# Optimization experiments

Measured on AMD Instinct MI355X. Metric: run time of the kernel, lower is better.

## Reference

```python
import jax, jax.numpy as jnp
import numpy as np

# Degree-sorted atom layout (DeepChem convention): atoms of degree d are contiguous.
D_COUNTS = [8192, 65536, 131072, 196608, 98304, 16384, 8192]  # degrees 0..6
OFFSETS = np.cumsum([0] + D_COUNTS)  # start index of each degree block
N_ATOMS = int(OFFSETS[-1])           # 524288
F_IN = 75
BATCH = 16384
MAX_DEG = 6
BN_EPS = 1e-3


def setup_inputs() -> dict:
    key = jax.random.key(0)
    ks = jax.random.split(key, 40)
    inp = {}
    inp["atom_features"] = jax.random.normal(ks[0], (N_ATOMS, F_IN), jnp.float32)
    # every molecule gets exactly N_ATOMS/BATCH atoms -> all segments populated
    inp["membership"] = (jnp.arange(N_ATOMS, dtype=jnp.int32) % BATCH)
    for d in range(1, MAX_DEG + 1):
        inp[f"adj{d}"] = jax.random.randint(ks[d], (D_COUNTS[d], d), 0, N_ATOMS, dtype=jnp.int32)
    # GraphConv weights: 2*MAX_DEG + 1 = 13 matrices (rel/self per degree 1..6, self for degree 0)
    inp["gc1_W"] = jax.random.normal(ks[10], (13, F_IN, 32), jnp.float32) * 0.1
    inp["gc1_b"] = jax.random.normal(ks[11], (13, 32), jnp.float32) * 0.01
    inp["gc2_W"] = jax.random.normal(ks[12], (13, 32, 32), jnp.float32) * 0.1
    inp["gc2_b"] = jax.random.normal(ks[13], (13, 32), jnp.float32) * 0.01
    inp["bn1_gamma"] = jnp.ones((32,), jnp.float32)
    inp["bn1_beta"] = jnp.zeros((32,), jnp.float32)
    inp["bn1_mean"] = jax.random.normal(ks[14], (32,), jnp.float32) * 0.1
    inp["bn1_var"] = jax.random.uniform(ks[15], (32,), jnp.float32, 0.5, 1.5)
    inp["bn3_gamma"] = jnp.ones((64,), jnp.float32)
    inp["bn3_beta"] = jnp.zeros((64,), jnp.float32)
    inp["bn3_mean"] = jax.random.normal(ks[16], (64,), jnp.float32) * 0.1
    inp["bn3_var"] = jax.random.uniform(ks[17], (64,), jnp.float32, 0.5, 1.5)
    inp["d1_W"] = jax.random.normal(ks[18], (32, 64), jnp.float32) * 0.1
    inp["d1_b"] = jnp.zeros((64,), jnp.float32)
    inp["d2_W"] = jax.random.normal(ks[19], (128, 1), jnp.float32) * 0.1
    inp["d2_b"] = jnp.zeros((1,), jnp.float32)
    inp["d3_W"] = jnp.array([0.5, -1, -1, 1, 1, 1, 1, 1, -1, -1, -1, -1, -1, -1, -1, -1], jnp.float32)[:, None]
    inp["d3_b"] = jnp.zeros((1,), jnp.float32)
    inp["x_add"] = jax.random.normal(ks[20], (BATCH, 15), jnp.float32)
    inp["batch_size"] = BATCH
    return inp


def _batch_norm(x, gamma, beta, mean, var):
    return gamma * (x - mean) * jax.lax.rsqrt(var + BN_EPS) + beta


def _graph_conv(atoms, adjs, W, b):
    # atoms: [N, F]; adjs[d-1]: [n_d, d] neighbor indices for degree-d atoms
    outs = []
    for d in range(1, MAX_DEG + 1):
        s, n = int(OFFSETS[d]), D_COUNTS[d]
        rel = atoms[adjs[d - 1]].sum(axis=1)          # [n_d, F] summed neighbors
        self_a = atoms[s:s + n]                        # [n_d, F]
        wr, br = W[2 * (d - 1)], b[2 * (d - 1)]
        ws, bs = W[2 * (d - 1) + 1], b[2 * (d - 1) + 1]
        outs.append(rel @ wr + br + self_a @ ws + bs)
    out0 = atoms[:D_COUNTS[0]] @ W[12] + b[12]         # degree-0: self only
    return jnp.tanh(jnp.concatenate([out0] + outs, axis=0))


def _graph_pool(atoms, adjs):
    outs = [atoms[:D_COUNTS[0]]]  # degree-0 passthrough
    for d in range(1, MAX_DEG + 1):
        s, n = int(OFFSETS[d]), D_COUNTS[d]
        self_a = atoms[s:s + n]
        neigh_max = atoms[adjs[d - 1]].max(axis=1)     # [n_d, F]
        outs.append(jnp.maximum(self_a, neigh_max))    # max over {self} U neighbors
    return jnp.concatenate(outs, axis=0)


def reference(atom_features, membership, adj1, adj2, adj3, adj4, adj5, adj6,
              gc1_W, gc1_b, gc2_W, gc2_b,
              bn1_gamma, bn1_beta, bn1_mean, bn1_var,
              bn3_gamma, bn3_beta, bn3_mean, bn3_var,
              d1_W, d1_b, d2_W, d2_b, d3_W, d3_b, x_add, batch_size):
    adjs = [adj1, adj2, adj3, adj4, adj5, adj6]
    h = _graph_conv(atom_features, adjs, gc1_W, gc1_b)          # [N, 32], tanh
    h = _batch_norm(h, bn1_gamma, bn1_beta, bn1_mean, bn1_var)
    h = _graph_pool(h, adjs)
    h = _graph_conv(h, adjs, gc2_W, gc2_b)                      # [N, 32]
    # NOTE: original reuses batch_norm1 here (source does self.batch_norm1 twice)
    h = _batch_norm(h, bn1_gamma, bn1_beta, bn1_mean, bn1_var)
    h = _graph_pool(h, adjs)
    h = jnp.tanh(h @ d1_W + d1_b)                               # [N, 64]
    h = _batch_norm(h, bn3_gamma, bn3_beta, bn3_mean, bn3_var)
    # GraphGather: per-molecule sum and max readout
    sum_r = jax.ops.segment_sum(h, membership, num_segments=batch_size)
    max_r = jax.ops.segment_max(h, membership, num_segments=batch_size)
    mol = jnp.tanh(jnp.concatenate([sum_r, max_r], axis=1))     # [B, 128]
    model_var = mol @ d2_W + d2_b                               # [B, 1]
    binding = jnp.concatenate([model_var, x_add], axis=1)       # [B, 16]
    ans = binding @ d3_W + d3_b                                 # [B, 1]
    return ans.reshape(1, -1)
```

## Files before the change

kernel.cpp:

```cpp
#include <hip/hip_runtime.h>

typedef unsigned short u16;
typedef __bf16 bf8v __attribute__((ext_vector_type(8)));
typedef float f32x4 __attribute__((ext_vector_type(4)));

#define N_ATOMS 524288
#define NROW32  16777216

#define P_EP1   0
#define P_EP2   224
#define P_BN1   448
#define P_BN3   576
#define P_D1WT  832
#define P_D1B   2880
#define P_D2W   2944
#define P_SC    3072

__device__ __forceinline__ float b2f(u16 u) {
  return __builtin_bit_cast(float, ((unsigned)u) << 16);
}
__device__ __forceinline__ u16 f2b(float f) {
  unsigned x = __builtin_bit_cast(unsigned, f);
  x += 0x7fffu + ((x >> 16) & 1u);
  return (u16)(x >> 16);
}
__device__ __forceinline__ float ldf(const void* p, size_t i, int isbf) {
  return isbf ? b2f(((const u16*)p)[i]) : ((const float*)p)[i];
}
__device__ __forceinline__ u16 ldb(const void* p, size_t i, int isbf) {
  return isbf ? ((const u16*)p)[i] : f2b(((const float*)p)[i]);
}

__device__ __forceinline__ float exp2_fast(float x) {
#if __has_builtin(__builtin_amdgcn_exp2f)
  return __builtin_amdgcn_exp2f(x);
#else
  return exp2f(x);
#endif
}
__device__ __forceinline__ float rcp_fast(float x) {
#if __has_builtin(__builtin_amdgcn_rcpf)
  return __builtin_amdgcn_rcpf(x);
#else
  return 1.0f / x;
#endif
}
__device__ __forceinline__ float tanh_fast(float x) {
  float xc = fminf(fmaxf(x, -15.f), 15.f);
  float t = exp2_fast(xc * -2.8853900817779268f);
  return (1.f - t) * rcp_fast(1.f + t);
}

__device__ __forceinline__ void seg_of(int r, int& d, int& off) {
  if      (r < 8192)   { d = 0; off = 0; }
  else if (r < 73728)  { d = 1; off = 8192; }
  else if (r < 204800) { d = 2; off = 73728; }
  else if (r < 401408) { d = 3; off = 204800; }
  else if (r < 499712) { d = 4; off = 401408; }
  else if (r < 516096) { d = 5; off = 499712; }
  else                 { d = 6; off = 516096; }
}

__global__ void probe_kernel(const void* __restrict__ atoms, int* __restrict__ flag) {
  int lane = threadIdx.x;
  unsigned u = ((const u16*)atoms)[(size_t)lane * 148];
  int e = (u >> 7) & 0xFF;
  bool ok = (e >= 100 && e <= 140);
  unsigned long long b = __ballot(ok);
  if (lane == 0) flag[0] = (__popcll(b) >= 48) ? 1 : 0;
}

__global__ __launch_bounds__(64) void prep_kernel(
    const void* gW1, const void* gB1, const void* gW2, const void* gB2,
    const void* b1g, const void* b1b, const void* b1m, const void* b1v,
    const void* g3, const void* b3, const void* m3, const void* v3,
    const void* d1W, const void* d1b, const void* d2W, const void* d2b,
    const void* d3W, const void* d3b,
    const int* flagp, char* ws)
{
  const int isbf = flagp[0];
  const int lane = threadIdx.x;
  float* P  = (float*)(ws + 256);
  u16* wf1 = (u16*)(ws + 16384);
  u16* wf2 = (u16*)(ws + 88064);
  const int blk = blockIdx.x;

  if (blk < 7) {
    const int d = blk;
    const int wr  = (d == 0) ? 12 : 2 * (d - 1);
    const int wsi = (d == 0) ? 12 : 2 * (d - 1) + 1;
    const int nl = lane & 15, q = lane >> 4;
    #pragma unroll
    for (int ks = 0; ks < 5; ++ks)
      #pragma unroll
      for (int ct = 0; ct < 2; ++ct) {
        u16* dst = wf1 + (size_t)(((d * 5 + ks) * 2 + ct) * 64 + lane) * 8;
        #pragma unroll
        for (int j = 0; j < 8; ++j) {
          int k = ks * 32 + q * 8 + j, n = ct * 16 + nl;
          u16 val = 0;
          if (k < 75) val = ldb(gW1, (size_t)wr * 2400 + k * 32 + n, isbf);
          else if (k >= 80 && k < 155) val = ldb(gW1, (size_t)wsi * 2400 + (k - 80) * 32 + n, isbf);
          dst[j] = val;
        }
      }
    #pragma unroll
    for (int ks = 0; ks < 2; ++ks)
      #pragma unroll
      for (int ct = 0; ct < 2; ++ct) {
        u16* dst = wf2 + (size_t)(((d * 2 + ks) * 2 + ct) * 64 + lane) * 8;
        #pragma unroll
        for (int j = 0; j < 8; ++j) {
          int k = ks * 32 + q * 8 + j, n = ct * 16 + nl;
          dst[j] = (k < 32) ? ldb(gW2, (size_t)wr * 1024 + k * 32 + n, isbf)
                            : ldb(gW2, (size_t)wsi * 1024 + (k - 32) * 32 + n, isbf);
        }
      }
    if (lane < 32) {
      int col = lane;
      float bb1 = (d == 0) ? ldf(gB1, 12 * 32 + col, isbf)
                           : ldf(gB1, wr * 32 + col, isbf) + ldf(gB1, wsi * 32 + col, isbf);
      float bb2 = (d == 0) ? ldf(gB2, 12 * 32 + col, isbf)
                           : ldf(gB2, wr * 32 + col, isbf) + ldf(gB2, wsi * 32 + col, isbf);
      P[P_EP1 + d * 32 + col] = bb1;
      P[P_EP2 + d * 32 + col] = bb2;
    }
  } else {
    if (lane < 32) {
      P[P_BN1 + lane]      = ldf(b1g, lane, isbf);
      P[P_BN1 + 32 + lane] = ldf(b1b, lane, isbf);
      P[P_BN1 + 64 + lane] = ldf(b1m, lane, isbf);
      P[P_BN1 + 96 + lane] = 1.0f / sqrtf(ldf(b1v, lane, isbf) + 0.001f);
    }
    P[P_BN3 + lane]       = ldf(g3, lane, isbf);
    P[P_BN3 + 64 + lane]  = ldf(b3, lane, isbf);
    P[P_BN3 + 128 + lane] = ldf(m3, lane, isbf);
    P[P_BN3 + 192 + lane] = 1.0f / sqrtf(ldf(v3, lane, isbf) + 0.001f);
    for (int k = 0; k < 32; ++k)
      P[P_D1WT + lane * 32 + k] = ldf(d1W, k * 64 + lane, isbf);
    P[P_D1B + lane] = ldf(d1b, lane, isbf);
    P[P_D2W + lane]      = ldf(d2W, lane, isbf);
    P[P_D2W + 64 + lane] = ldf(d2W, 64 + lane, isbf);
    if (lane < 16) P[P_SC + 1 + lane] = ldf(d3W, lane, isbf);
    if (lane == 0) { P[P_SC] = ldf(d2b, 0, isbf); P[P_SC + 17] = ldf(d3b, 0, isbf); }
  }
}

__global__ __launch_bounds__(256) void convert_kernel(
    const void* __restrict__ atoms, const int* flagp, u16* __restrict__ outB)
{
  __shared__ __align__(16) u16 sT[128 * 80];
  const int isbf = flagp[0];
  const int tid = threadIdx.x;
  const int rb = blockIdx.x * 128;

  for (int i = tid; i < 128 * 5; i += 256) {
    int rl = i / 5, k = 75 + (i % 5);
    sT[rl * 80 + k] = 0;
  }
  if (isbf) {
    const uint4* in4 = (const uint4*)((const u16*)atoms + (size_t)rb * 75);
    for (int i = tid; i < 1200; i += 256) {
      union { uint4 u4; u16 us[8]; } w; w.u4 = in4[i];
      int e0 = i * 8;
      #pragma unroll
      for (int j = 0; j < 8; ++j) {
        int e = e0 + j, rl = e / 75, k = e - rl * 75;
        sT[rl * 80 + k] = w.us[j];
      }
    }
  } else {
    const f32x4* in4 = (const f32x4*)((const float*)atoms + (size_t)rb * 75);
    for (int i = tid; i < 2400; i += 256) {
      f32x4 v = in4[i];
      int e0 = i * 4;
      #pragma unroll
      for (int j = 0; j < 4; ++j) {
        int e = e0 + j, rl = e / 75, k = e - rl * 75;
        sT[rl * 80 + k] = f2b(v[j]);
      }
    }
  }
  __syncthreads();
  uint4* dst = (uint4*)(outB + (size_t)rb * 80);
  const uint4* src = (const uint4*)sT;
  for (int i = tid; i < 1280; i += 256) dst[i] = src[i];
}

template<int D>
__device__ __forceinline__ void gather2_conv1(
    const u16* __restrict__ atomsB, const int* __restrict__ adjp,
    int r0, int r1, int off, int q, bf8v a0[5], bf8v a1[5])
{
  constexpr int DD = (D > 0) ? D : 1;
  int nb0[DD], nb1[DD];
  if (D > 0) {
    size_t i0 = (size_t)(r0 - off) * D, i1 = (size_t)(r1 - off) * D;
    #pragma unroll
    for (int j = 0; j < D; ++j) { nb0[j] = adjp[i0 + j]; nb1[j] = adjp[i1 + j]; }
  }
  const u16* s0 = atomsB + (size_t)r0 * 80;
  const u16* s1 = atomsB + (size_t)r1 * 80;
  #pragma unroll
  for (int ks = 0; ks < 5; ++ks) {
    const int c = ks * 32 + q * 8;
    if (c >= 80) {
      a0[ks] = *(const bf8v*)(s0 + (c - 80));
      a1[ks] = *(const bf8v*)(s1 + (c - 80));
    } else {
      uint4 v0[DD], v1[DD];
      #pragma unroll
      for (int j = 0; j < D; ++j) {
        v0[j] = *(const uint4*)(atomsB + (size_t)nb0[j] * 80 + c);
        v1[j] = *(const uint4*)(atomsB + (size_t)nb1[j] * 80 + c);
      }
      float r0s[8], r1s[8];
      #pragma unroll
      for (int i = 0; i < 8; ++i) { r0s[i] = 0.f; r1s[i] = 0.f; }
      #pragma unroll
      for (int j = 0; j < D; ++j) {
        union { uint4 u4; u16 us[8]; } a, b;
        a.u4 = v0[j]; b.u4 = v1[j];
        #pragma unroll
        for (int i = 0; i < 8; ++i) { r0s[i] += b2f(a.us[i]); r1s[i] += b2f(b.us[i]); }
      }
      union { u16 us[8]; bf8v v; } o0, o1;
      #pragma unroll
      for (int i = 0; i < 8; ++i) { o0.us[i] = f2b(r0s[i]); o1.us[i] = f2b(r1s[i]); }
      a0[ks] = o0.v; a1[ks] = o1.v;
    }
  }
}

__global__ __launch_bounds__(256) void conv1_fast_kernel(
    const u16* __restrict__ atomsB, const u16* __restrict__ wf1, const float* __restrict__ P,
    const int* __restrict__ a1p, const int* __restrict__ a2p, const int* __restrict__ a3p,
    const int* __restrict__ a4p, const int* __restrict__ a5p, const int* __restrict__ a6p,
    u16* __restrict__ out)
{
  const int tid = threadIdx.x;
  const int rb = blockIdx.x * 128;
  int d, off; seg_of(rb, d, off);
  const int lane = tid & 63;
  const int nl = lane & 15;
  const int q  = lane >> 4;
  const int wvid = tid >> 6;

  bf8v bfrag[5][2];
  #pragma unroll
  for (int ks = 0; ks < 5; ++ks)
    #pragma unroll
    for (int ct = 0; ct < 2; ++ct)
      bfrag[ks][ct] = *(const bf8v*)(wf1 + (size_t)(((d * 5 + ks) * 2 + ct) * 64 + lane) * 8);

  const int r0 = rb + wvid * 32 + nl;
  const int r1 = r0 + 16;
  bf8v a0[5], a1f[5];
  switch (d) {
    case 0: gather2_conv1<0>(atomsB, a1p, r0, r1, off, q, a0, a1f); break;
    case 1: gather2_conv1<1>(atomsB, a1p, r0, r1, off, q, a0, a1f); break;
    case 2: gather2_conv1<2>(atomsB, a2p, r0, r1, off, q, a0, a1f); break;
    case 3: gather2_conv1<3>(atomsB, a3p, r0, r1, off, q, a0, a1f); break;
    case 4: gather2_conv1<4>(atomsB, a4p, r0, r1, off, q, a0, a1f); break;
    case 5: gather2_conv1<5>(atomsB, a5p, r0, r1, off, q, a0, a1f); break;
    default: gather2_conv1<6>(atomsB, a6p, r0, r1, off, q, a0, a1f); break;
  }

  f32x4 acc[2][2] = {{{0,0,0,0},{0,0,0,0}},{{0,0,0,0},{0,0,0,0}}};
  #pragma unroll
  for (int ks = 0; ks < 5; ++ks) {
    acc[0][0] = __builtin_amdgcn_mfma_f32_16x16x32_bf16(a0[ks],  bfrag[ks][0], acc[0][0], 0, 0, 0);
    acc[0][1] = __builtin_amdgcn_mfma_f32_16x16x32_bf16(a0[ks],  bfrag[ks][1], acc[0][1], 0, 0, 0);
    acc[1][0] = __builtin_amdgcn_mfma_f32_16x16x32_bf16(a1f[ks], bfrag[ks][0], acc[1][0], 0, 0, 0);
    acc[1][1] = __builtin_amdgcn_mfma_f32_16x16x32_bf16(a1f[ks], bfrag[ks][1], acc[1][1], 0, 0, 0);
  }

  #pragma unroll
  for (int ct = 0; ct < 2; ++ct) {
    const int col = ct * 16 + nl;
    const float bias = P[P_EP1 + d * 32 + col];
    const float g  = P[P_BN1 + col];
    const float be = P[P_BN1 + 32 + col];
    const float mn = P[P_BN1 + 64 + col];
    const float iv = P[P_BN1 + 96 + col];
    #pragma unroll
    for (int t = 0; t < 2; ++t) {
      #pragma unroll
      for (int reg = 0; reg < 4; ++reg) {
        int row = rb + wvid * 32 + t * 16 + q * 4 + reg;
        float v = tanh_fast(acc[t][ct][reg] + bias);
        out[(size_t)row * 32 + col] = f2b(g * (v - mn) * iv + be);
      }
    }
  }
}

__global__ __launch_bounds__(256) void conv1_slow_kernel(
    const void* __restrict__ atoms, const void* __restrict__ gW, const void* __restrict__ gB,
    const void* __restrict__ bng, const void* __restrict__ bnb,
    const void* __restrict__ bnm, const void* __restrict__ bnv,
    const int* __restrict__ a1, const int* __restrict__ a2, const int* __restrict__ a3,
    const int* __restrict__ a4, const int* __restrict__ a5, const int* __restrict__ a6,
    const int* flagp, u16* __restrict__ out)
{
  __shared__ __align__(16) u16 sX[64 * 168];
  const int isbf = flagp[0];
  const int tid = threadIdx.x;
  const int rb = blockIdx.x * 64;
  int d, off; seg_of(rb, d, off);
  const int wr  = (d == 0) ? 12 : 2 * (d - 1);
  const int wsi = (d == 0) ? 12 : 2 * (d - 1) + 1;
  const size_t wrb = (size_t)wr  * 2400;
  const size_t wsb = (size_t)wsi * 2400;
  const int lane = tid & 63;
  const int nl = lane & 15;
  const int q  = lane >> 4;

  bf8v bfrag[5][2];
  #pragma unroll
  for (int ks = 0; ks < 5; ++ks)
    #pragma unroll
    for (int ct = 0; ct < 2; ++ct) {
      union { u16 u[8]; bf8v v; } tmp;
      #pragma unroll
      for (int j = 0; j < 8; ++j) {
        int k = ks * 32 + q * 8 + j, n = ct * 16 + nl;
        u16 val = 0;
        if (k < 75) val = ldb(gW, wrb + (size_t)k * 32 + n, isbf);
        else if (k >= 80 && k < 155) val = ldb(gW, wsb + (size_t)(k - 80) * 32 + n, isbf);
        tmp.u[j] = val;
      }
      bfrag[ks][ct] = tmp.v;
    }

  {
    const int lr = tid >> 2;
    const int kq = tid & 3;
    const int r  = rb + lr;
    int nb[6];
    if (d > 0) {
      const int* adjp = (d==1)?a1:(d==2)?a2:(d==3)?a3:(d==4)?a4:(d==5)?a5:a6;
      size_t ib = (size_t)(r - off) * d;
      for (int j = 0; j < d; ++j) nb[j] = adjp[ib + j];
    }
    u16* px = sX + lr * 168;
    for (int k = kq; k < 80; k += 4) {
      u16 sv = 0; float rs = 0.f;
      if (k < 75) {
        sv = ldb(atoms, (size_t)r * 75 + k, isbf);
        for (int j = 0; j < d; ++j) rs += ldf(atoms, (size_t)nb[j] * 75 + k, isbf);
      }
      px[80 + k] = sv;
      px[k]      = f2b(rs);
    }
  }
  __syncthreads();

  const int wvid = tid >> 6;
  f32x4 acc0 = {0.f, 0.f, 0.f, 0.f};
  f32x4 acc1 = {0.f, 0.f, 0.f, 0.f};
  const u16* abase = sX + (wvid * 16 + nl) * 168 + q * 8;
  #pragma unroll
  for (int ks = 0; ks < 5; ++ks) {
    bf8v a = *(const bf8v*)(abase + ks * 32);
    acc0 = __builtin_amdgcn_mfma_f32_16x16x32_bf16(a, bfrag[ks][0], acc0, 0, 0, 0);
    acc1 = __builtin_amdgcn_mfma_f32_16x16x32_bf16(a, bfrag[ks][1], acc1, 0, 0, 0);
  }
  #pragma unroll
  for (int ct = 0; ct < 2; ++ct) {
    f32x4 acc = ct ? acc1 : acc0;
    int col = ct * 16 + nl;
    float bias = (d == 0) ? ldf(gB, 12 * 32 + col, isbf)
                          : ldf(gB, wr * 32 + col, isbf) + ldf(gB, wsi * 32 + col, isbf);
    float g  = ldf(bng, col, isbf);
    float be = ldf(bnb, col, isbf);
    float mn = ldf(bnm, col, isbf);
    float iv = 1.0f / sqrtf(ldf(bnv, col, isbf) + 0.001f);
    #pragma unroll
    for (int reg = 0; reg < 4; ++reg) {
      int row = rb + wvid * 16 + q * 4 + reg;
      float t = tanh_fast(acc[reg] + bias);
      out[(size_t)row * 32 + col] = f2b(g * (t - mn) * iv + be);
    }
  }
}

template<int D>
__device__ __forceinline__ void gather2_conv2(
    const u16* __restrict__ in, const int* __restrict__ adjp,
    int r0, int r1, int off, int q, bf8v a0[2], bf8v a1[2])
{
  constexpr int DD = (D > 0) ? D : 1;
  int nb0[DD], nb1[DD];
  if (D > 0) {
    size_t i0 = (size_t)(r0 - off) * D, i1 = (size_t)(r1 - off) * D;
    #pragma unroll
    for (int j = 0; j < D; ++j) { nb0[j] = adjp[i0 + j]; nb1[j] = adjp[i1 + j]; }
  }
  a0[1] = *(const bf8v*)(in + (size_t)r0 * 32 + q * 8);
  a1[1] = *(const bf8v*)(in + (size_t)r1 * 32 + q * 8);
  uint4 v0[DD], v1[DD];
  #pragma unroll
  for (int j = 0; j < D; ++j) {
    v0[j] = *(const uint4*)(in + (size_t)nb0[j] * 32 + q * 8);
    v1[j] = *(const uint4*)(in + (size_t)nb1[j] * 32 + q * 8);
  }
  float r0s[8], r1s[8];
  #pragma unroll
  for (int i = 0; i < 8; ++i) { r0s[i] = 0.f; r1s[i] = 0.f; }
  #pragma unroll
  for (int j = 0; j < D; ++j) {
    union { uint4 u4; u16 us[8]; } a, b;
    a.u4 = v0[j]; b.u4 = v1[j];
    #pragma unroll
    for (int i = 0; i < 8; ++i) { r0s[i] += b2f(a.us[i]); r1s[i] += b2f(b.us[i]); }
  }
  union { u16 us[8]; bf8v v; } o0, o1;
  #pragma unroll
  for (int i = 0; i < 8; ++i) { o0.us[i] = f2b(r0s[i]); o1.us[i] = f2b(r1s[i]); }
  a0[0] = o0.v; a1[0] = o1.v;
}

__global__ __launch_bounds__(256) void conv2_kernel(
    const u16* __restrict__ in, const u16* __restrict__ wf2, const float* __restrict__ P,
    const int* __restrict__ a1p, const int* __restrict__ a2p, const int* __restrict__ a3p,
    const int* __restrict__ a4p, const int* __restrict__ a5p, const int* __restrict__ a6p,
    u16* __restrict__ out)
{
  const int tid = threadIdx.x;
  const int rb = blockIdx.x * 128;
  int d, off; seg_of(rb, d, off);
  const int lane = tid & 63;
  const int nl = lane & 15;
  const int q  = lane >> 4;
  const int wvid = tid >> 6;

  bf8v bfrag[2][2];
  #pragma unroll
  for (int ks = 0; ks < 2; ++ks)
    #pragma unroll
    for (int ct = 0; ct < 2; ++ct)
      bfrag[ks][ct] = *(const bf8v*)(wf2 + (size_t)(((d * 2 + ks) * 2 + ct) * 64 + lane) * 8);

  const int r0 = rb + wvid * 32 + nl;
  const int r1 = r0 + 16;
  bf8v a0[2], a1f[2];
  switch (d) {
    case 0: gather2_conv2<0>(in, a1p, r0, r1, off, q, a0, a1f); break;
    case 1: gather2_conv2<1>(in, a1p, r0, r1, off, q, a0, a1f); break;
    case 2: gather2_conv2<2>(in, a2p, r0, r1, off, q, a0, a1f); break;
    case 3: gather2_conv2<3>(in, a3p, r0, r1, off, q, a0, a1f); break;
    case 4: gather2_conv2<4>(in, a4p, r0, r1, off, q, a0, a1f); break;
    case 5: gather2_conv2<5>(in, a5p, r0, r1, off, q, a0, a1f); break;
    default: gather2_conv2<6>(in, a6p, r0, r1, off, q, a0, a1f); break;
  }

  f32x4 acc[2][2] = {{{0,0,0,0},{0,0,0,0}},{{0,0,0,0},{0,0,0,0}}};
  #pragma unroll
  for (int ks = 0; ks < 2; ++ks) {
    acc[0][0] = __builtin_amdgcn_mfma_f32_16x16x32_bf16(a0[ks],  bfrag[ks][0], acc[0][0], 0, 0, 0);
    acc[0][1] = __builtin_amdgcn_mfma_f32_16x16x32_bf16(a0[ks],  bfrag[ks][1], acc[0][1], 0, 0, 0);
    acc[1][0] = __builtin_amdgcn_mfma_f32_16x16x32_bf16(a1f[ks], bfrag[ks][0], acc[1][0], 0, 0, 0);
    acc[1][1] = __builtin_amdgcn_mfma_f32_16x16x32_bf16(a1f[ks], bfrag[ks][1], acc[1][1], 0, 0, 0);
  }

  #pragma unroll
  for (int ct = 0; ct < 2; ++ct) {
    const int col = ct * 16 + nl;
    const float bias = P[P_EP2 + d * 32 + col];
    const float g  = P[P_BN1 + col];
    const float be = P[P_BN1 + 32 + col];
    const float mn = P[P_BN1 + 64 + col];
    const float iv = P[P_BN1 + 96 + col];
    #pragma unroll
    for (int t = 0; t < 2; ++t) {
      #pragma unroll
      for (int reg = 0; reg < 4; ++reg) {
        int row = rb + wvid * 32 + t * 16 + q * 4 + reg;
        float v = tanh_fast(acc[t][ct][reg] + bias);
        out[(size_t)row * 32 + col] = f2b(g * (v - mn) * iv + be);
      }
    }
  }
}

template<int D>
__device__ __forceinline__ void pool_one(
    const u16* __restrict__ in, const int* __restrict__ adjp,
    int r, int off, int q8, u16* __restrict__ out)
{
  constexpr int DD = (D > 0) ? D : 1;
  int nb[DD];
  if (D > 0) {
    size_t ib = (size_t)(r - off) * D;
    #pragma unroll
    for (int j = 0; j < D; ++j) nb[j] = adjp[ib + j];
  }
  uint4 sv = *(const uint4*)(in + (size_t)r * 32 + q8);
  uint4 nv[DD];
  #pragma unroll
  for (int j = 0; j < D; ++j) nv[j] = *(const uint4*)(in + (size_t)nb[j] * 32 + q8);
  union { uint4 u4; u16 us[8]; } s; s.u4 = sv;
  float v[8];
  #pragma unroll
  for (int i = 0; i < 8; ++i) v[i] = b2f(s.us[i]);
  #pragma unroll
  for (int j = 0; j < D; ++j) {
    union { uint4 u4; u16 us[8]; } a; a.u4 = nv[j];
    #pragma unroll
    for (int i = 0; i < 8; ++i) v[i] = fmaxf(v[i], b2f(a.us[i]));
  }
  union { uint4 u4; u16 us[8]; } o;
  #pragma unroll
  for (int i = 0; i < 8; ++i) o.us[i] = f2b(v[i]);
  *(uint4*)(out + (size_t)r * 32 + q8) = o.u4;
}

__global__ __launch_bounds__(256) void pool_kernel(
    const u16* __restrict__ in, u16* __restrict__ out,
    const int* __restrict__ a1, const int* __restrict__ a2, const int* __restrict__ a3,
    const int* __restrict__ a4, const int* __restrict__ a5, const int* __restrict__ a6)
{
  int idx = blockIdx.x * 256 + threadIdx.x;
  int r = idx >> 2, q8 = (idx & 3) * 8;
  int d, off; seg_of(r, d, off);
  switch (d) {
    case 0: pool_one<0>(in, a1, r, off, q8, out); break;
    case 1: pool_one<1>(in, a1, r, off, q8, out); break;
    case 2: pool_one<2>(in, a2, r, off, q8, out); break;
    case 3: pool_one<3>(in, a3, r, off, q8, out); break;
    case 4: pool_one<4>(in, a4, r, off, q8, out); break;
    case 5: pool_one<5>(in, a5, r, off, q8, out); break;
    default: pool_one<6>(in, a6, r, off, q8, out); break;
  }
}

__global__ __launch_bounds__(256) void head_kernel(
    const u16* __restrict__ in, const float* __restrict__ P,
    const void* __restrict__ xadd, const int* flagp, void* __restrict__ outp)
{
  __shared__ __align__(16) float sA[4][1024];
  const int isbf = flagp[0];
  const int wvid = threadIdx.x >> 6;
  const int m = blockIdx.x * 4 + wvid;
  const int j = threadIdx.x & 63;

  #pragma unroll
  for (int ii = 0; ii < 2; ++ii) {
    int i = j + ii * 64;
    int t = i >> 2, kq8 = (i & 3) * 8;
    union { uint4 u4; u16 us[8]; } w;
    w.u4 = *(const uint4*)(in + (size_t)(m + t * 16384) * 32 + kq8);
    #pragma unroll
    for (int x = 0; x < 8; ++x) sA[wvid][t * 32 + kq8 + x] = b2f(w.us[x]);
  }
  __syncthreads();

  float wcol[32];
  const f32x4* wt4 = (const f32x4*)(P + P_D1WT + j * 32);
  #pragma unroll
  for (int k4 = 0; k4 < 8; ++k4) {
    f32x4 w4 = wt4[k4];
    wcol[k4 * 4] = w4[0]; wcol[k4 * 4 + 1] = w4[1];
    wcol[k4 * 4 + 2] = w4[2]; wcol[k4 * 4 + 3] = w4[3];
  }
  const float bj = P[P_D1B + j];
  const float g  = P[P_BN3 + j];
  const float bt = P[P_BN3 + 64 + j];
  const float mn = P[P_BN3 + 128 + j];
  const float iv = P[P_BN3 + 192 + j];

  float sum = 0.f, mx = -1e30f;
  for (int t = 0; t < 32; ++t) {
    const f32x4* arow = (const f32x4*)(&sA[wvid][t * 32]);
    float dot = bj;
    #pragma unroll
    for (int k4 = 0; k4 < 8; ++k4) {
      f32x4 av = arow[k4];
      dot += av[0] * wcol[k4 * 4]     + av[1] * wcol[k4 * 4 + 1]
           + av[2] * wcol[k4 * 4 + 2] + av[3] * wcol[k4 * 4 + 3];
    }
    float h  = tanh_fast(dot);
    float hb = g * (h - mn) * iv + bt;
    sum += hb;
    mx = fmaxf(mx, hb);
  }

  float part = tanh_fast(sum) * P[P_D2W + j] + tanh_fast(mx) * P[P_D2W + 64 + j];
  #pragma unroll
  for (int o = 32; o > 0; o >>= 1) part += __shfl_down(part, o, 64);

  if (j == 0) {
    float mv  = part + P[P_SC];
    float ans = mv * P[P_SC + 1] + P[P_SC + 17];
    #pragma unroll
    for (int i = 0; i < 15; ++i) ans += ldf(xadd, m * 15 + i, isbf) * P[P_SC + 2 + i];
    if (isbf) ((u16*)outp)[m] = f2b(ans);
    else      ((float*)outp)[m] = ans;
  }
}

extern "C" void kernel_launch(void* const* d_in, const int* in_sizes, int n_in,
                              void* d_out, int out_size, void* d_ws, size_t ws_size,
                              hipStream_t stream)
{
  (void)in_sizes; (void)n_in; (void)out_size;
  const void* atoms = d_in[0];
  const int* a1 = (const int*)d_in[2];
  const int* a2 = (const int*)d_in[3];
  const int* a3 = (const int*)d_in[4];
  const int* a4 = (const int*)d_in[5];
  const int* a5 = (const int*)d_in[6];
  const int* a6 = (const int*)d_in[7];

  char* ws = (char*)d_ws;
  int*  flag = (int*)ws;
  float* P   = (float*)(ws + 256);
  u16*  wf1  = (u16*)(ws + 16384);
  u16*  wf2  = (u16*)(ws + 88064);
  u16*  buf0 = (u16*)(ws + 131072);

  const size_t need = 131072 + (size_t)NROW32 * 2 + (size_t)N_ATOMS * 80 * 2;
  const bool fast = ws_size >= need;

  probe_kernel<<<1, 64, 0, stream>>>(atoms, flag);
  prep_kernel<<<8, 64, 0, stream>>>(d_in[8], d_in[9], d_in[10], d_in[11],
                                    d_in[12], d_in[13], d_in[14], d_in[15],
                                    d_in[16], d_in[17], d_in[18], d_in[19],
                                    d_in[20], d_in[21], d_in[22], d_in[23],
                                    d_in[24], d_in[25], flag, ws);

  u16* buf1;
  if (fast) {
    u16* atomsB = buf0 + NROW32;
    buf1 = atomsB;
    convert_kernel<<<4096, 256, 0, stream>>>(atoms, flag, atomsB);
    conv1_fast_kernel<<<4096, 256, 0, stream>>>(atomsB, wf1, P,
                                                a1, a2, a3, a4, a5, a6, buf0);
  } else {
    buf1 = buf0 + NROW32;
    conv1_slow_kernel<<<8192, 256, 0, stream>>>(atoms, d_in[8], d_in[9], d_in[12],
                                                d_in[13], d_in[14], d_in[15],
                                                a1, a2, a3, a4, a5, a6, flag, buf0);
  }

  pool_kernel<<<8192, 256, 0, stream>>>(buf0, buf1, a1, a2, a3, a4, a5, a6);
  conv2_kernel<<<4096, 256, 0, stream>>>(buf1, wf2, P, a1, a2, a3, a4, a5, a6, buf0);
  pool_kernel<<<8192, 256, 0, stream>>>(buf0, buf1, a1, a2, a3, a4, a5, a6);
  head_kernel<<<4096, 256, 0, stream>>>(buf1, P, d_in[26], flag, d_out);
}
```

Baseline: 556.5 us.

## Project atoms per weight before gathering in conv1, fuse final pool into head

Conv1 now runs in two stages. First, every atom's 75-wide features are multiplied by all seven relevant weight matrices, giving seven 32-wide bf16 tables. Second, neighbour rows of these tables are gathered and summed, so each neighbour read is 64 bytes instead of a full 160-byte feature row. The second graph pool is folded into the head kernel, batch-norm is folded into a precomputed scale and shift, and the dtype probe is merged into the prep kernel, which together remove kernel launches and one full pass over the activations. In exchange, conv1 writes and reads about 235 MB of projection tables and needs a much larger workspace, falling back to the slow path when the workspace is too small.

```diff
diff --git a/kernel.cpp b/kernel.cpp
--- a/kernel.cpp
+++ b/kernel.cpp
@@ -7,14 +7,23 @@
 #define N_ATOMS 524288
 #define NROW32  16777216
 
+#define WS_P      256
+#define WS_WF1    16384
+#define WS_WF2    98304
+#define WS_BUF0   131072
+#define WS_ATOMSB (131072 + 33554432)
+#define WS_PROJ   (WS_ATOMSB + 83886080)
+#define WS_NEED_FAST ((size_t)WS_PROJ + (size_t)7 * NROW32 * 2)
+
 #define P_EP1   0
 #define P_EP2   224
-#define P_BN1   448
-#define P_BN3   576
-#define P_D1WT  832
-#define P_D1B   2880
-#define P_D2W   2944
-#define P_SC    3072
+#define P_BN1A  448
+#define P_BN1B  480
+#define P_BN3   512
+#define P_D1WT  768
+#define P_D1B   2816
+#define P_D2W   2880
+#define P_SC    3008
 
 __device__ __forceinline__ float b2f(u16 u) {
   return __builtin_bit_cast(float, ((unsigned)u) << 16);
@@ -61,28 +70,22 @@
   else                 { d = 6; off = 516096; }
 }
 
-__global__ void probe_kernel(const void* __restrict__ atoms, int* __restrict__ flag) {
-  int lane = threadIdx.x;
-  unsigned u = ((const u16*)atoms)[(size_t)lane * 148];
-  int e = (u >> 7) & 0xFF;
-  bool ok = (e >= 100 && e <= 140);
-  unsigned long long b = __ballot(ok);
-  if (lane == 0) flag[0] = (__popcll(b) >= 48) ? 1 : 0;
-}
-
 __global__ __launch_bounds__(64) void prep_kernel(
+    const void* atoms,
     const void* gW1, const void* gB1, const void* gW2, const void* gB2,
     const void* b1g, const void* b1b, const void* b1m, const void* b1v,
     const void* g3, const void* b3, const void* m3, const void* v3,
     const void* d1W, const void* d1b, const void* d2W, const void* d2b,
-    const void* d3W, const void* d3b,
-    const int* flagp, char* ws)
-{
-  const int isbf = flagp[0];
+    const void* d3W, const void* d3b, char* ws)
+{
   const int lane = threadIdx.x;
-  float* P  = (float*)(ws + 256);
-  u16* wf1 = (u16*)(ws + 16384);
-  u16* wf2 = (u16*)(ws + 88064);
+  unsigned u = ((const u16*)atoms)[(size_t)lane * 148];
+  int e = (u >> 7) & 0xFF;
+  const int isbf = (__popcll(__ballot(e >= 100 && e <= 140)) >= 48) ? 1 : 0;
+
+  float* P  = (float*)(ws + WS_P);
+  u16* wf1 = (u16*)(ws + WS_WF1);
+  u16* wf2 = (u16*)(ws + WS_WF2);
   const int blk = blockIdx.x;
 
   if (blk < 7) {
@@ -90,20 +93,22 @@
     const int wr  = (d == 0) ? 12 : 2 * (d - 1);
     const int wsi = (d == 0) ? 12 : 2 * (d - 1) + 1;
     const int nl = lane & 15, q = lane >> 4;
-    #pragma unroll
-    for (int ks = 0; ks < 5; ++ks)
-      #pragma unroll
-      for (int ct = 0; ct < 2; ++ct) {
-        u16* dst = wf1 + (size_t)(((d * 5 + ks) * 2 + ct) * 64 + lane) * 8;
+    int mlist[2]; int nm;
+    if (d == 0) { mlist[0] = 12; nm = 1; } else { mlist[0] = wr; mlist[1] = wsi; nm = 2; }
+    for (int mi = 0; mi < nm; ++mi) {
+      int m = mlist[mi];
+      #pragma unroll
+      for (int ks = 0; ks < 3; ++ks)
         #pragma unroll
-        for (int j = 0; j < 8; ++j) {
-          int k = ks * 32 + q * 8 + j, n = ct * 16 + nl;
-          u16 val = 0;
-          if (k < 75) val = ldb(gW1, (size_t)wr * 2400 + k * 32 + n, isbf);
-          else if (k >= 80 && k < 155) val = ldb(gW1, (size_t)wsi * 2400 + (k - 80) * 32 + n, isbf);
-          dst[j] = val;
+        for (int ct = 0; ct < 2; ++ct) {
+          u16* dst = wf1 + (size_t)(((m * 3 + ks) * 2 + ct) * 64 + lane) * 8;
+          #pragma unroll
+          for (int j = 0; j < 8; ++j) {
+            int k = ks * 32 + q * 8 + j, n = ct * 16 + nl;
+            dst[j] = (k < 75) ? ldb(gW1, (size_t)m * 2400 + k * 32 + n, isbf) : (u16)0;
+          }
         }
-      }
+    }
     #pragma unroll
     for (int ks = 0; ks < 2; ++ks)
       #pragma unroll
@@ -116,21 +121,25 @@
                             : ldb(gW2, (size_t)wsi * 1024 + (k - 32) * 32 + n, isbf);
         }
       }
+  } else {
+    if (lane == 0) ((int*)ws)[0] = isbf;
     if (lane < 32) {
-      int col = lane;
-      float bb1 = (d == 0) ? ldf(gB1, 12 * 32 + col, isbf)
-                           : ldf(gB1, wr * 32 + col, isbf) + ldf(gB1, wsi * 32 + col, isbf);
-      float bb2 = (d == 0) ? ldf(gB2, 12 * 32 + col, isbf)
-                           : ldf(gB2, wr * 32 + col, isbf) + ldf(gB2, wsi * 32 + col, isbf);
-      P[P_EP1 + d * 32 + col] = bb1;
-      P[P_EP2 + d * 32 + col] = bb2;
-    }
-  } else {
-    if (lane < 32) {
-      P[P_BN1 + lane]      = ldf(b1g, lane, isbf);
-      P[P_BN1 + 32 + lane] = ldf(b1b, lane, isbf);
-      P[P_BN1 + 64 + lane] = ldf(b1m, lane, isbf);
-      P[P_BN1 + 96 + lane] = 1.0f / sqrtf(ldf(b1v, lane, isbf) + 0.001f);
+      for (int d = 0; d < 7; ++d) {
+        int wr  = (d == 0) ? 12 : 2 * (d - 1);
+        int wsi = (d == 0) ? 12 : 2 * (d - 1) + 1;
+        float bb1 = (d == 0) ? ldf(gB1, 12 * 32 + lane, isbf)
+                             : ldf(gB1, wr * 32 + lane, isbf) + ldf(gB1, wsi * 32 + lane, isbf);
+        float bb2 = (d == 0) ? ldf(gB2, 12 * 32 + lane, isbf)
+                             : ldf(gB2, wr * 32 + lane, isbf) + ldf(gB2, wsi * 32 + lane, isbf);
+        P[P_EP1 + d * 32 + lane] = bb1;
+        P[P_EP2 + d * 32 + lane] = bb2;
+      }
+      float g  = ldf(b1g, lane, isbf);
+      float be = ldf(b1b, lane, isbf);
+      float mn = ldf(b1m, lane, isbf);
+      float iv = 1.0f / sqrtf(ldf(b1v, lane, isbf) + 0.001f);
+      P[P_BN1A + lane] = g * iv;
+      P[P_BN1B + lane] = be - mn * g * iv;
     }
     P[P_BN3 + lane]       = ldf(g3, lane, isbf);
     P[P_BN3 + 64 + lane]  = ldf(b3, lane, isbf);
@@ -187,111 +196,111 @@
   for (int i = tid; i < 1280; i += 256) dst[i] = src[i];
 }
 
-template<int D>
-__device__ __forceinline__ void gather2_conv1(
-    const u16* __restrict__ atomsB, const int* __restrict__ adjp,
-    int r0, int r1, int off, int q, bf8v a0[5], bf8v a1[5])
-{
-  constexpr int DD = (D > 0) ? D : 1;
-  int nb0[DD], nb1[DD];
-  if (D > 0) {
-    size_t i0 = (size_t)(r0 - off) * D, i1 = (size_t)(r1 - off) * D;
-    #pragma unroll
-    for (int j = 0; j < D; ++j) { nb0[j] = adjp[i0 + j]; nb1[j] = adjp[i1 + j]; }
-  }
-  const u16* s0 = atomsB + (size_t)r0 * 80;
-  const u16* s1 = atomsB + (size_t)r1 * 80;
-  #pragma unroll
-  for (int ks = 0; ks < 5; ++ks) {
-    const int c = ks * 32 + q * 8;
-    if (c >= 80) {
-      a0[ks] = *(const bf8v*)(s0 + (c - 80));
-      a1[ks] = *(const bf8v*)(s1 + (c - 80));
-    } else {
-      uint4 v0[DD], v1[DD];
-      #pragma unroll
-      for (int j = 0; j < D; ++j) {
-        v0[j] = *(const uint4*)(atomsB + (size_t)nb0[j] * 80 + c);
-        v1[j] = *(const uint4*)(atomsB + (size_t)nb1[j] * 80 + c);
-      }
-      float r0s[8], r1s[8];
-      #pragma unroll
-      for (int i = 0; i < 8; ++i) { r0s[i] = 0.f; r1s[i] = 0.f; }
-      #pragma unroll
-      for (int j = 0; j < D; ++j) {
-        union { uint4 u4; u16 us[8]; } a, b;
-        a.u4 = v0[j]; b.u4 = v1[j];
-        #pragma unroll
-        for (int i = 0; i < 8; ++i) { r0s[i] += b2f(a.us[i]); r1s[i] += b2f(b.us[i]); }
-      }
-      union { u16 us[8]; bf8v v; } o0, o1;
-      #pragma unroll
-      for (int i = 0; i < 8; ++i) { o0.us[i] = f2b(r0s[i]); o1.us[i] = f2b(r1s[i]); }
-      a0[ks] = o0.v; a1[ks] = o1.v;
-    }
-  }
-}
-
-__global__ __launch_bounds__(256) void conv1_fast_kernel(
-    const u16* __restrict__ atomsB, const u16* __restrict__ wf1, const float* __restrict__ P,
-    const int* __restrict__ a1p, const int* __restrict__ a2p, const int* __restrict__ a3p,
-    const int* __restrict__ a4p, const int* __restrict__ a5p, const int* __restrict__ a6p,
-    u16* __restrict__ out)
+__global__ __launch_bounds__(256) void projA_kernel(
+    const u16* __restrict__ atomsB, const u16* __restrict__ wf1,
+    const float* __restrict__ P, u16* __restrict__ proj)
 {
   const int tid = threadIdx.x;
-  const int rb = blockIdx.x * 128;
+  const int rb = blockIdx.x * 64;
   int d, off; seg_of(rb, d, off);
+  const int wsi = (d == 0) ? 12 : 2 * (d - 1) + 1;
   const int lane = tid & 63;
   const int nl = lane & 15;
   const int q  = lane >> 4;
-  const int wvid = tid >> 6;
-
-  bf8v bfrag[5][2];
-  #pragma unroll
-  for (int ks = 0; ks < 5; ++ks)
-    #pragma unroll
-    for (int ct = 0; ct < 2; ++ct)
-      bfrag[ks][ct] = *(const bf8v*)(wf1 + (size_t)(((d * 5 + ks) * 2 + ct) * 64 + lane) * 8);
-
-  const int r0 = rb + wvid * 32 + nl;
-  const int r1 = r0 + 16;
-  bf8v a0[5], a1f[5];
+  const int w  = tid >> 6;
+
+  const u16* rowp = atomsB + (size_t)(rb + w * 16 + nl) * 80;
+  bf8v af[3];
+  af[0] = *(const bf8v*)(rowp + q * 8);
+  af[1] = *(const bf8v*)(rowp + 32 + q * 8);
+  {
+    int c2 = 64 + q * 8;
+    if (c2 < 80) af[2] = *(const bf8v*)(rowp + c2);
+    else { union { u16 us[8]; bf8v v; } z = {}; af[2] = z.v; }
+  }
+
+  #pragma unroll
+  for (int t = 0; t < 7; ++t) {
+    const int m = (t == 0) ? wsi : 2 * (t - 1);
+    u16* outp = proj + (size_t)t * NROW32;
+    f32x4 acc0 = {0.f, 0.f, 0.f, 0.f};
+    f32x4 acc1 = {0.f, 0.f, 0.f, 0.f};
+    #pragma unroll
+    for (int ks = 0; ks < 3; ++ks) {
+      bf8v b0 = *(const bf8v*)(wf1 + (size_t)(((m * 3 + ks) * 2 + 0) * 64 + lane) * 8);
+      bf8v b1 = *(const bf8v*)(wf1 + (size_t)(((m * 3 + ks) * 2 + 1) * 64 + lane) * 8);
+      acc0 = __builtin_amdgcn_mfma_f32_16x16x32_bf16(af[ks], b0, acc0, 0, 0, 0);
+      acc1 = __builtin_amdgcn_mfma_f32_16x16x32_bf16(af[ks], b1, acc1, 0, 0, 0);
+    }
+    #pragma unroll
+    for (int ct = 0; ct < 2; ++ct) {
+      const int col = ct * 16 + nl;
+      const float bias = (t == 0) ? P[P_EP1 + d * 32 + col] : 0.f;
+      f32x4 a = ct ? acc1 : acc0;
+      #pragma unroll
+      for (int reg = 0; reg < 4; ++reg) {
+        int row = rb + w * 16 + q * 4 + reg;
+        outp[(size_t)row * 32 + col] = f2b(a[reg] + bias);
+      }
+    }
+  }
+}
+
+template<int D>
+__device__ __forceinline__ void gatherB_one(
+    const u16* __restrict__ proj, const int* __restrict__ adjp,
+    int r, int off, int q8, const float* __restrict__ P, u16* __restrict__ out)
+{
+  union { uint4 u4; u16 us[8]; } s;
+  s.u4 = *(const uint4*)(proj + (size_t)r * 32 + q8);
+  float v[8];
+  #pragma unroll
+  for (int i = 0; i < 8; ++i) v[i] = b2f(s.us[i]);
+  if (D > 0) {
+    const u16* Pd = proj + (size_t)D * NROW32;
+    int nb[D > 0 ? D : 1];
+    size_t ib = (size_t)(r - off) * D;
+    #pragma unroll
+    for (int j = 0; j < D; ++j) nb[j] = adjp[ib + j];
+    uint4 nv[D > 0 ? D : 1];
+    #pragma unroll
+    for (int j = 0; j < D; ++j) nv[j] = *(const uint4*)(Pd + (size_t)nb[j] * 32 + q8);
+    #pragma unroll
+    for (int j = 0; j < D; ++j) {
+      union { uint4 u4; u16 us[8]; } a; a.u4 = nv[j];
+      #pragma unroll
+      for (int i = 0; i < 8; ++i) v[i] += b2f(a.us[i]);
+    }
+  }
+  f32x4 A0 = *(const f32x4*)(P + P_BN1A + q8);
+  f32x4 A1 = *(const f32x4*)(P + P_BN1A + q8 + 4);
+  f32x4 B0 = *(const f32x4*)(P + P_BN1B + q8);
+  f32x4 B1 = *(const f32x4*)(P + P_BN1B + q8 + 4);
+  union { uint4 u4; u16 us[8]; } o;
+  #pragma unroll
+  for (int i = 0; i < 4; ++i) o.us[i]     = f2b(A0[i] * tanh_fast(v[i])     + B0[i]);
+  #pragma unroll
+  for (int i = 0; i < 4; ++i) o.us[4 + i] = f2b(A1[i] * tanh_fast(v[4 + i]) + B1[i]);
+  *(uint4*)(out + (size_t)r * 32 + q8) = o.u4;
+}
+
+__global__ __launch_bounds__(256) void gatherB_kernel(
+    const u16* __restrict__ proj, const float* __restrict__ P,
+    const int* __restrict__ a1, const int* __restrict__ a2, const int* __restrict__ a3,
+    const int* __restrict__ a4, const int* __restrict__ a5, const int* __restrict__ a6,
+    u16* __restrict__ out)
+{
+  int idx = blockIdx.x * 256 + threadIdx.x;
+  int r = idx >> 2, q8 = (idx & 3) * 8;
+  int d, off; seg_of(r, d, off);
   switch (d) {
-    case 0: gather2_conv1<0>(atomsB, a1p, r0, r1, off, q, a0, a1f); break;
-    case 1: gather2_conv1<1>(atomsB, a1p, r0, r1, off, q, a0, a1f); break;
-    case 2: gather2_conv1<2>(atomsB, a2p, r0, r1, off, q, a0, a1f); break;
-    case 3: gather2_conv1<3>(atomsB, a3p, r0, r1, off, q, a0, a1f); break;
-    case 4: gather2_conv1<4>(atomsB, a4p, r0, r1, off, q, a0, a1f); break;
-    case 5: gather2_conv1<5>(atomsB, a5p, r0, r1, off, q, a0, a1f); break;
-    default: gather2_conv1<6>(atomsB, a6p, r0, r1, off, q, a0, a1f); break;
-  }
-
-  f32x4 acc[2][2] = {{{0,0,0,0},{0,0,0,0}},{{0,0,0,0},{0,0,0,0}}};
-  #pragma unroll
-  for (int ks = 0; ks < 5; ++ks) {
-    acc[0][0] = __builtin_amdgcn_mfma_f32_16x16x32_bf16(a0[ks],  bfrag[ks][0], acc[0][0], 0, 0, 0);
-    acc[0][1] = __builtin_amdgcn_mfma_f32_16x16x32_bf16(a0[ks],  bfrag[ks][1], acc[0][1], 0, 0, 0);
-    acc[1][0] = __builtin_amdgcn_mfma_f32_16x16x32_bf16(a1f[ks], bfrag[ks][0], acc[1][0], 0, 0, 0);
-    acc[1][1] = __builtin_amdgcn_mfma_f32_16x16x32_bf16(a1f[ks], bfrag[ks][1], acc[1][1], 0, 0, 0);
-  }
-
-  #pragma unroll
-  for (int ct = 0; ct < 2; ++ct) {
-    const int col = ct * 16 + nl;
-    const float bias = P[P_EP1 + d * 32 + col];
-    const float g  = P[P_BN1 + col];
-    const float be = P[P_BN1 + 32 + col];
-    const float mn = P[P_BN1 + 64 + col];
-    const float iv = P[P_BN1 + 96 + col];
-    #pragma unroll
-    for (int t = 0; t < 2; ++t) {
-      #pragma unroll
-      for (int reg = 0; reg < 4; ++reg) {
-        int row = rb + wvid * 32 + t * 16 + q * 4 + reg;
-        float v = tanh_fast(acc[t][ct][reg] + bias);
-        out[(size_t)row * 32 + col] = f2b(g * (v - mn) * iv + be);
-      }
-    }
+    case 0: gatherB_one<0>(proj, a1, r, off, q8, P, out); break;
+    case 1: gatherB_one<1>(proj, a1, r, off, q8, P, out); break;
+    case 2: gatherB_one<2>(proj, a2, r, off, q8, P, out); break;
+    case 3: gatherB_one<3>(proj, a3, r, off, q8, P, out); break;
+    case 4: gatherB_one<4>(proj, a4, r, off, q8, P, out); break;
+    case 5: gatherB_one<5>(proj, a5, r, off, q8, P, out); break;
+    default: gatherB_one<6>(proj, a6, r, off, q8, P, out); break;
   }
 }
 
@@ -468,17 +477,14 @@
   for (int ct = 0; ct < 2; ++ct) {
     const int col = ct * 16 + nl;
     const float bias = P[P_EP2 + d * 32 + col];
-    const float g  = P[P_BN1 + col];
-    const float be = P[P_BN1 + 32 + col];
-    const float mn = P[P_BN1 + 64 + col];
-    const float iv = P[P_BN1 + 96 + col];
+    const float A = P[P_BN1A + col];
+    const float B = P[P_BN1B + col];
     #pragma unroll
     for (int t = 0; t < 2; ++t) {
       #pragma unroll
       for (int reg = 0; reg < 4; ++reg) {
         int row = rb + wvid * 32 + t * 16 + q * 4 + reg;
-        float v = tanh_fast(acc[t][ct][reg] + bias);
-        out[(size_t)row * 32 + col] = f2b(g * (v - mn) * iv + be);
+        out[(size_t)row * 32 + col] = f2b(A * tanh_fast(acc[t][ct][reg] + bias) + B);
       }
     }
   }
@@ -537,6 +543,8 @@
 
 __global__ __launch_bounds__(256) void head_kernel(
     const u16* __restrict__ in, const float* __restrict__ P,
+    const int* __restrict__ a1, const int* __restrict__ a2, const int* __restrict__ a3,
+    const int* __restrict__ a4, const int* __restrict__ a5, const int* __restrict__ a6,
     const void* __restrict__ xadd, const int* flagp, void* __restrict__ outp)
 {
   __shared__ __align__(16) float sA[4][1024];
@@ -548,11 +556,29 @@
   #pragma unroll
   for (int ii = 0; ii < 2; ++ii) {
     int i = j + ii * 64;
-    int t = i >> 2, kq8 = (i & 3) * 8;
-    union { uint4 u4; u16 us[8]; } w;
-    w.u4 = *(const uint4*)(in + (size_t)(m + t * 16384) * 32 + kq8);
-    #pragma unroll
-    for (int x = 0; x < 8; ++x) sA[wvid][t * 32 + kq8 + x] = b2f(w.us[x]);
+    int t = i >> 2, q8 = (i & 3) * 8;
+    int r = m + t * 16384;
+    int d, off; seg_of(r, d, off);
+    const int* adjp = (d <= 1) ? a1 : (d == 2) ? a2 : (d == 3) ? a3
+                    : (d == 4) ? a4 : (d == 5) ? a5 : a6;
+    size_t ib = (size_t)(r - off) * (size_t)d;
+    union { uint4 u4; u16 us[8]; } s;
+    s.u4 = *(const uint4*)(in + (size_t)r * 32 + q8);
+    float v[8];
+    #pragma unroll
+    for (int x = 0; x < 8; ++x) v[x] = b2f(s.us[x]);
+    #pragma unroll
+    for (int jj = 0; jj < 6; ++jj) {
+      if (jj < d) {
+        int nb = adjp[ib + jj];
+        union { uint4 u4; u16 us[8]; } a;
+        a.u4 = *(const uint4*)(in + (size_t)nb * 32 + q8);
+        #pragma unroll
+        for (int x = 0; x < 8; ++x) v[x] = fmaxf(v[x], b2f(a.us[x]));
+      }
+    }
+    #pragma unroll
+    for (int x = 0; x < 8; ++x) sA[wvid][t * 32 + q8 + x] = v[x];
   }
   __syncthreads();
 
@@ -615,37 +641,37 @@
 
   char* ws = (char*)d_ws;
   int*  flag = (int*)ws;
-  float* P   = (float*)(ws + 256);
-  u16*  wf1  = (u16*)(ws + 16384);
-  u16*  wf2  = (u16*)(ws + 88064);
-  u16*  buf0 = (u16*)(ws + 131072);
-
-  const size_t need = 131072 + (size_t)NROW32 * 2 + (size_t)N_ATOMS * 80 * 2;
-  const bool fast = ws_size >= need;
-
-  probe_kernel<<<1, 64, 0, stream>>>(atoms, flag);
-  prep_kernel<<<8, 64, 0, stream>>>(d_in[8], d_in[9], d_in[10], d_in[11],
-                                    d_in[12], d_in[13], d_in[14], d_in[15],
-                                    d_in[16], d_in[17], d_in[18], d_in[19],
-                                    d_in[20], d_in[21], d_in[22], d_in[23],
-                                    d_in[24], d_in[25], flag, ws);
-
-  u16* buf1;
+  float* P   = (float*)(ws + WS_P);
+  u16*  wf1  = (u16*)(ws + WS_WF1);
+  u16*  wf2  = (u16*)(ws + WS_WF2);
+  u16*  buf0 = (u16*)(ws + WS_BUF0);
+  u16*  atomsB = (u16*)(ws + WS_ATOMSB);
+  u16*  proj = (u16*)(ws + WS_PROJ);
+
+  const bool fast = ws_size >= WS_NEED_FAST;
+
+  prep_kernel<<<8, 64, 0, stream>>>(atoms,
+      d_in[8], d_in[9], d_in[10], d_in[11],
+      d_in[12], d_in[13], d_in[14], d_in[15],
+      d_in[16], d_in[17], d_in[18], d_in[19],
+      d_in[20], d_in[21], d_in[22], d_in[23],
+      d_in[24], d_in[25], ws);
+
   if (fast) {
-    u16* atomsB = buf0 + NROW32;
-    buf1 = atomsB;
     convert_kernel<<<4096, 256, 0, stream>>>(atoms, flag, atomsB);
-    conv1_fast_kernel<<<4096, 256, 0, stream>>>(atomsB, wf1, P,
-                                                a1, a2, a3, a4, a5, a6, buf0);
+    projA_kernel<<<8192, 256, 0, stream>>>(atomsB, wf1, P, proj);
+    gatherB_kernel<<<8192, 256, 0, stream>>>(proj, P, a1, a2, a3, a4, a5, a6, buf0);
+    pool_kernel<<<8192, 256, 0, stream>>>(buf0, atomsB, a1, a2, a3, a4, a5, a6);
+    conv2_kernel<<<4096, 256, 0, stream>>>(atomsB, wf2, P, a1, a2, a3, a4, a5, a6, buf0);
   } else {
-    buf1 = buf0 + NROW32;
+    u16* buf1 = buf0 + NROW32;
     conv1_slow_kernel<<<8192, 256, 0, stream>>>(atoms, d_in[8], d_in[9], d_in[12],
                                                 d_in[13], d_in[14], d_in[15],
                                                 a1, a2, a3, a4, a5, a6, flag, buf0);
-  }
-
-  pool_kernel<<<8192, 256, 0, stream>>>(buf0, buf1, a1, a2, a3, a4, a5, a6);
-  conv2_kernel<<<4096, 256, 0, stream>>>(buf1, wf2, P, a1, a2, a3, a4, a5, a6, buf0);
-  pool_kernel<<<8192, 256, 0, stream>>>(buf0, buf1, a1, a2, a3, a4, a5, a6);
-  head_kernel<<<4096, 256, 0, stream>>>(buf1, P, d_in[26], flag, d_out);
-}
+    pool_kernel<<<8192, 256, 0, stream>>>(buf0, buf1, a1, a2, a3, a4, a5, a6);
+    conv2_kernel<<<4096, 256, 0, stream>>>(buf1, wf2, P, a1, a2, a3, a4, a5, a6, buf0);
+  }
+
+  head_kernel<<<4096, 256, 0, stream>>>(buf0, P, a1, a2, a3, a4, a5, a6,
+                                        d_in[26], flag, d_out);
+}
```

Result: slower. 591.9 us (+6.4%).
